# Kernel optimization log

Hardware: AMD Instinct MI355X
Metric: run time of the kernel (lower is better)

The kernel has to match this reference:

```python
import math
import jax, jax.numpy as jnp
import numpy as np

T, D = 1024, 7168
N = 128
A_Q, A_KV = 1536, 512
QK_NOPE, QK_ROPE, V_DIM = 128, 64, 128
QK_HEAD = QK_NOPE + QK_ROPE  # 192
PAD_H = 256                  # padded to multiple of 128 in attn_op
EPS = 1e-6
ROPE_THETA, FACTOR, ORIG_MAX = 10000.0, 40.0, 4096
BETA_FAST, BETA_SLOW = 32, 1


def _yarn_inv_freq():
    """DeepseekScalingRotaryEmbedding (yarn) inverse frequencies, static."""
    dim = QK_ROPE
    pos_freqs = ROPE_THETA ** (np.arange(0, dim, 2, dtype=np.float64) / dim)
    inv_extra = 1.0 / pos_freqs
    inv_inter = 1.0 / (FACTOR * pos_freqs)

    def corr_dim(n_rot):
        return dim * math.log(ORIG_MAX / (n_rot * 2 * math.pi)) / (2 * math.log(ROPE_THETA))

    low = max(math.floor(corr_dim(BETA_FAST)), 0)
    high = min(math.ceil(corr_dim(BETA_SLOW)), dim - 1)
    ramp = np.clip((np.arange(dim // 2, dtype=np.float64) - low) / max(high - low, 1e-3), 0.0, 1.0)
    mask = 1.0 - ramp  # 1 -> extrapolation, 0 -> interpolation
    inv = inv_inter * (1.0 - mask) + inv_extra * mask
    return jnp.asarray(inv, dtype=jnp.float32)

_INV_FREQ = _yarn_inv_freq()
# mscale ratio: yarn_get_mscale(FACTOR, mscale)/yarn_get_mscale(FACTOR, mscale_all_dim) == 1.0
_MSCALE = 1.0


def _apply_rope(positions, x):
    # x: [T, N, QK_ROPE], split (rotate-half) ordering
    ang = positions[:, None].astype(jnp.float32) * _INV_FREQ[None, :]  # [T, 32]
    cos = (jnp.cos(ang) * _MSCALE)[:, None, :]
    sin = (jnp.sin(ang) * _MSCALE)[:, None, :]
    x1, x2 = x[..., : QK_ROPE // 2], x[..., QK_ROPE // 2:]
    return jnp.concatenate([x1 * cos - x2 * sin, x2 * cos + x1 * sin], axis=-1)


def _rms_norm(x, scale):
    var = jnp.mean(x * x, axis=-1, keepdims=True)
    return x * jax.lax.rsqrt(var + EPS) * scale


def setup_inputs() -> dict:
    key = jax.random.key(0)
    ks = jax.random.split(key, 6)
    s = 0.02
    return {
        "x": jax.random.normal(ks[0], (T, D), jnp.float32),
        "positions": jnp.arange(T, dtype=jnp.int32),
        "w_q_down": jax.random.normal(ks[1], (D, A_Q), jnp.float32) * s,
        "q_norm_scale": jnp.ones((A_Q,), jnp.float32),
        "w_q_up": jax.random.normal(ks[2], (A_Q, N, QK_HEAD), jnp.float32) * s,
        "w_kv_down": jax.random.normal(ks[3], (D, A_KV + QK_ROPE), jnp.float32) * s,
        "kv_norm_scale": jnp.ones((A_KV,), jnp.float32),
        "w_kv_up": jax.random.normal(ks[4], (A_KV, N, QK_NOPE + V_DIM), jnp.float32) * s,
        "w_o": jax.random.normal(ks[5], (N, V_DIM, D), jnp.float32) * s,
    }


def reference(x, positions, w_q_down, q_norm_scale, w_q_up, w_kv_down,
              kv_norm_scale, w_kv_up, w_o):
    # ---- q path: down-proj -> RMSNorm -> up-proj -> split RoPE ----
    q_TA = jnp.einsum('td,da->ta', x, w_q_down)
    q_TA = _rms_norm(q_TA, q_norm_scale)
    q_TNH = jnp.einsum('ta,anh->tnh', q_TA, w_q_up)
    q_rope = _apply_rope(positions, q_TNH[..., QK_NOPE:])
    q_TNH = jnp.concatenate([q_TNH[..., :QK_NOPE], q_rope], axis=-1)
    q_TNH = q_TNH * (QK_HEAD ** -0.5)

    # ---- kv path: down-proj -> (rope slice | RMSNorm latent -> up-proj) ----
    kv_SA = jnp.einsum('sd,da->sa', x, w_kv_down)
    k_rope = _apply_rope(positions, kv_SA[..., A_KV:][:, None, :])  # [S,1,64]
    k_rope = jnp.broadcast_to(k_rope, (T, N, QK_ROPE))
    c_SA = _rms_norm(kv_SA[..., :A_KV], kv_norm_scale)
    kv_nope = jnp.einsum('sa,anh->snh', c_SA, w_kv_up)
    k_SNH = jnp.concatenate([kv_nope[..., :QK_NOPE], k_rope], axis=-1)
    v_SNH = kv_nope[..., QK_NOPE:]

    # ---- attention (prefill, causal); zero-pad of head dim does not change dots,
    # but sm_scale uses the PADDED dim (256) as in the original attn_op ----
    sm_scale = PAD_H ** -0.5
    logits = jnp.einsum('tnh,snh->nts', q_TNH, k_SNH) * sm_scale
    t_idx = jnp.arange(T)
    causal = t_idx[:, None] >= t_idx[None, :]  # [T, S]
    logits = jnp.where(causal[None, :, :], logits, jnp.float32(-1e30))
    probs = jax.nn.softmax(logits, axis=-1)
    out_TNH = jnp.einsum('nts,snh->tnh', probs, v_SNH)

    # ---- output projection ----
    o_TD = jnp.einsum('tnh,nhd->td', out_TNH, w_o)
    return o_TD
```

## Files before the change

### kernel.cpp

```cpp
#include <hip/hip_runtime.h>
#include <hip/hip_bf16.h>
#include <math.h>

typedef __attribute__((ext_vector_type(4))) float f32x4;
typedef __attribute__((ext_vector_type(8))) short bf16x8;
typedef __attribute__((ext_vector_type(4))) short bf16x4;

static __device__ __forceinline__ float bf2f(short u){
  unsigned int i = ((unsigned int)(unsigned short)u) << 16;
  return __builtin_bit_cast(float, i);
}
static __device__ __forceinline__ short f2bf(float f){
  unsigned int u = __builtin_bit_cast(unsigned int, f);
  u += 0x7FFFu + ((u >> 16) & 1u);
  return (short)(u >> 16);
}

#define GLD16(g, l) __builtin_amdgcn_global_load_lds(                         \
    (const __attribute__((address_space(1))) void*)(g),                       \
    (__attribute__((address_space(3))) void*)(l), 16, 0, 0)

template<typename CT, int SPLITS>
__global__ __launch_bounds__(512, 2) void gemm256(const short* __restrict__ A,
                                                  const short* __restrict__ BT,
                                                  CT* __restrict__ C,
                                                  float* __restrict__ P,
                                                  int M, int N, int K)
{
  extern __shared__ __align__(16) char smem[];
  const int tid = threadIdx.x;
  const int w = tid >> 6, lane = tid & 63;
  const int wm = w >> 2, wn = w & 3;
  const int g = lane >> 4, l16 = lane & 15;

  const int per_z = gridDim.x * gridDim.y;
  const int F = (blockIdx.z * gridDim.y + blockIdx.y) * gridDim.x + blockIdx.x;
  const int nwgF = per_z * gridDim.z;
  const int cpxF = nwgF >> 3;
  const int T = (F & 7) * cpxF + (F >> 3);
  const int zz = T / per_z, tt = T % per_z;
  const int m0 = (tt & 3) * 256;
  const int n0 = (tt >> 2) * 256;

  const int Ks   = K / SPLITS;
  const int kbeg = zz * Ks;
  const int NT   = Ks >> 5;

  const int gg = (lane & 3) ^ ((lane >> 2) & 3) ^ ((lane >> 4) & 1);
  const short* aSrc[2]; const short* bSrc[2];
  int ldsOff[2];
  #pragma unroll
  for (int j = 0; j < 2; j++){
    int r = (w + j*8)*16 + (lane >> 2);
    aSrc[j] = A  + (size_t)(m0 + r) * K + kbeg + gg*8;
    bSrc[j] = BT + (size_t)(n0 + r) * K + kbeg + gg*8;
    ldsOff[j] = (w + j*8) * 1024;
  }

  const int sw = ((g ^ (l16 & 3) ^ ((l16 >> 2) & 1)) << 4);

  f32x4 acc[8][4];
  #pragma unroll
  for (int i = 0; i < 8; i++)
    #pragma unroll
    for (int j = 0; j < 4; j++) acc[i][j] = (f32x4){0.f,0.f,0.f,0.f};

  auto stage = [&](int b, int t){
    const int koff = t * 32;
    char* dst = smem + b * 32768;
    #pragma unroll
    for (int j = 0; j < 2; j++){
      GLD16(aSrc[j] + koff, dst + ldsOff[j]);
      GLD16(bSrc[j] + koff, dst + 16384 + ldsOff[j]);
    }
  };

  auto wait_pub = [&](int ahead){
    if (ahead >= 3)      asm volatile("s_waitcnt vmcnt(8)" ::: "memory");
    else if (ahead == 2) asm volatile("s_waitcnt vmcnt(4)" ::: "memory");
    else                 asm volatile("s_waitcnt vmcnt(0)" ::: "memory");
    __builtin_amdgcn_s_barrier();
    asm volatile("" ::: "memory");
  };

  stage(0, 0);
  if (NT > 1) stage(1, 1);
  if (NT > 2) stage(2, 2);
  wait_pub(NT - 1 >= 2 ? (NT > 2 ? 3 : 2) : 1);

  const int arow = wm*128 + l16;
  const int brow = wn*64  + l16;

  for (int t = 0; t < NT; t++){
    const int sl = t & 3;
    if (t + 3 < NT) stage((t + 3) & 3, t + 3);

    const char* base = smem + sl * 32768;
    bf16x8 a[8], bb[4];
    #pragma unroll
    for (int mi = 0; mi < 8; mi++)
      a[mi] = *reinterpret_cast<const bf16x8*>(base + (arow + mi*16)*64 + sw);
    #pragma unroll
    for (int ni = 0; ni < 4; ni++)
      bb[ni] = *reinterpret_cast<const bf16x8*>(base + 16384 + (brow + ni*16)*64 + sw);

    __builtin_amdgcn_s_setprio(1);
    #pragma unroll
    for (int mi = 0; mi < 8; mi++)
      #pragma unroll
      for (int ni = 0; ni < 4; ni++)
        acc[mi][ni] = __builtin_amdgcn_mfma_f32_16x16x32_bf16(a[mi], bb[ni], acc[mi][ni], 0, 0, 0);
    __builtin_amdgcn_s_setprio(0);

    wait_pub(NT - 1 - t);
  }

  #pragma unroll
  for (int mi = 0; mi < 8; mi++){
    int row = m0 + wm*128 + mi*16 + g*4;
    #pragma unroll
    for (int ni = 0; ni < 4; ni++){
      int col = n0 + wn*64 + ni*16 + l16;
      #pragma unroll
      for (int r = 0; r < 4; r++){
        if constexpr (SPLITS > 1){
          P[(size_t)zz*M*N + (size_t)(row+r)*N + col] = acc[mi][ni][r];
        } else if constexpr (sizeof(CT) == 4){
          C[(size_t)(row+r)*N + col] = acc[mi][ni][r];
        } else {
          C[(size_t)(row+r)*N + col] = f2bf(acc[mi][ni][r]);
        }
      }
    }
  }
}

template<typename CT, int SPLITS>
__global__ __launch_bounds__(256) void gemm_bt(const short* __restrict__ A,
                                               const short* __restrict__ BT,
                                               CT* __restrict__ C,
                                               float* __restrict__ P,
                                               int M, int N, int K)
{
  __shared__ __align__(16) short As[2][128*32];
  __shared__ __align__(16) short Bs[2][128*32];
  const int tid = threadIdx.x;
  const int f   = blockIdx.y * 8 + blockIdx.x;
  const int nwg = 8 * gridDim.y;
  const int cpx = nwg >> 3;
  const int t   = (f & 7) * cpx + (f >> 3);
  const int m0  = (t & 7) * 128;
  const int n0  = (t >> 3) * 128;
  const int w = tid >> 6, lane = tid & 63;
  const int wr = w >> 1, wc = w & 1;
  const int g = lane >> 4, l16 = lane & 15;

  const int Ks   = K / SPLITS;
  const int kbeg = blockIdx.z * Ks;
  const int kend = kbeg + Ks;

  const int sr = lane >> 2;
  const int kc = (lane & 3) << 3;
  const int arow0 = m0 + w*16 + sr;
  const int arow1 = m0 + (w+4)*16 + sr;
  int brow0 = n0 + w*16 + sr;      if (brow0 >= N) brow0 = N - 1;
  int brow1 = n0 + (w+4)*16 + sr;  if (brow1 >= N) brow1 = N - 1;
  const short* aG0 = A  + (size_t)arow0 * K + kc;
  const short* aG1 = A  + (size_t)arow1 * K + kc;
  const short* bG0 = BT + (size_t)brow0 * K + kc;
  const short* bG1 = BT + (size_t)brow1 * K + kc;
  char* aL = (char*)As;
  char* bL = (char*)Bs;

  auto stage = [&](int buf, int k0){
    char* ab = aL + buf*8192;
    char* bb = bL + buf*8192;
    GLD16(aG0 + k0, ab + (w  )*1024);
    GLD16(aG1 + k0, ab + (w+4)*1024);
    GLD16(bG0 + k0, bb + (w  )*1024);
    GLD16(bG1 + k0, bb + (w+4)*1024);
  };

  f32x4 acc[4][4];
  #pragma unroll
  for (int i=0;i<4;i++)
    #pragma unroll
    for (int j=0;j<4;j++) acc[i][j] = (f32x4){0.f,0.f,0.f,0.f};

  stage(0, kbeg);
  __syncthreads();

  int cur = 0;
  for (int k0 = kbeg; k0 < kend; k0 += 32){
    if (k0 + 32 < kend) stage(cur ^ 1, k0 + 32);

    const char* ar = aL + cur*8192;
    const char* br = bL + cur*8192;
    bf16x8 af[4], bfm[4];
    #pragma unroll
    for (int mi=0;mi<4;mi++){
      int row = wr*64 + mi*16 + l16;
      af[mi] = *reinterpret_cast<const bf16x8*>(ar + row*64 + g*16);
    }
    #pragma unroll
    for (int ni=0;ni<4;ni++){
      int row = wc*64 + ni*16 + l16;
      bfm[ni] = *reinterpret_cast<const bf16x8*>(br + row*64 + g*16);
    }
    #pragma unroll
    for (int mi=0;mi<4;mi++)
      #pragma unroll
      for (int ni=0;ni<4;ni++)
        acc[mi][ni] = __builtin_amdgcn_mfma_f32_16x16x32_bf16(af[mi], bfm[ni], acc[mi][ni], 0, 0, 0);

    __syncthreads();
    cur ^= 1;
  }

  #pragma unroll
  for (int mi=0;mi<4;mi++){
    int row = m0 + wr*64 + mi*16 + g*4;
    #pragma unroll
    for (int ni=0;ni<4;ni++){
      int col = n0 + wc*64 + ni*16 + l16;
      if (col < N){
        #pragma unroll
        for (int r=0;r<4;r++){
          if constexpr (SPLITS > 1){
            P[(size_t)blockIdx.z*M*N + (size_t)(row+r)*N + col] = acc[mi][ni][r];
          } else if constexpr (sizeof(CT) == 4){
            C[(size_t)(row+r)*N + col] = acc[mi][ni][r];
          } else {
            C[(size_t)(row+r)*N + col] = f2bf(acc[mi][ni][r]);
          }
        }
      }
    }
  }
}

template<int NP>
__global__ __launch_bounds__(256) void reduceN(const float* __restrict__ p,
                                               float* __restrict__ out,
                                               int n4, int mn4)
{
  int i = blockIdx.x * 256 + threadIdx.x;
  const int stride = gridDim.x * 256;
  for (; i < n4; i += stride){
    f32x4 s = reinterpret_cast<const f32x4*>(p)[i];
    #pragma unroll
    for (int z = 1; z < NP; z++)
      s = s + reinterpret_cast<const f32x4*>(p)[(size_t)z*mn4 + i];
    reinterpret_cast<f32x4*>(out)[i] = s;
  }
}

__global__ __launch_bounds__(256) void transpose_f32_bf16(const float* __restrict__ src,
                                                          short* __restrict__ dst,
                                                          int R, int C)
{
  __shared__ float tl[64][68];
  const int tid = threadIdx.x;
  const int r0 = blockIdx.y * 64, c0 = blockIdx.x * 64;
  {
    const int lr = tid >> 4, lc = (tid & 15) << 2;
    #pragma unroll
    for (int p = 0; p < 4; p++){
      int row = p*16 + lr;
      f32x4 v = *reinterpret_cast<const f32x4*>(src + (size_t)(r0+row)*C + c0 + lc);
      *reinterpret_cast<f32x4*>(&tl[row][lc]) = v;
    }
  }
  __syncthreads();
  {
    const int n = tid >> 2, ks = (tid & 3) << 4;
    short tmp[16];
    #pragma unroll
    for (int j = 0; j < 16; j++) tmp[j] = f2bf(tl[ks + j][n]);
    short* d = dst + (size_t)(c0+n)*R + r0 + ks;
    *reinterpret_cast<bf16x8*>(d)     = *reinterpret_cast<bf16x8*>(&tmp[0]);
    *reinterpret_cast<bf16x8*>(d + 8) = *reinterpret_cast<bf16x8*>(&tmp[8]);
  }
}

__global__ __launch_bounds__(256) void conv_f32_bf16(const float* __restrict__ src,
                                                     short* __restrict__ dst, int n4)
{
  int i = blockIdx.x * 256 + threadIdx.x;
  const int stride = gridDim.x * 256;
  for (; i < n4; i += stride){
    f32x4 v = reinterpret_cast<const f32x4*>(src)[i];
    bf16x4 h; h[0]=f2bf(v[0]); h[1]=f2bf(v[1]); h[2]=f2bf(v[2]); h[3]=f2bf(v[3]);
    reinterpret_cast<bf16x4*>(dst)[i] = h;
  }
}

__global__ __launch_bounds__(256) void mla_rmsnorm_bf(const float* __restrict__ dc,
                                                      const float* __restrict__ scale,
                                                      short* __restrict__ out)
{
  const int t = blockIdx.x;
  const float* row = dc + (size_t)t * 2112;
  float ss = 0.f;
  for (int i = threadIdx.x; i < 1536; i += 256){ float v = row[i]; ss += v*v; }
  #pragma unroll
  for (int off = 32; off >= 1; off >>= 1) ss += __shfl_xor(ss, off);
  __shared__ float red[4];
  if ((threadIdx.x & 63) == 0) red[threadIdx.x >> 6] = ss;
  __syncthreads();
  ss = red[0] + red[1] + red[2] + red[3];
  const float rs = 1.0f / sqrtf(ss / 1536.f + 1e-6f);
  for (int i = threadIdx.x; i < 1536; i += 256)
    out[(size_t)t*1536 + i] = f2bf(row[i] * rs * scale[i]);
}

__device__ __forceinline__ void yarn_cs(int pos, int j, float& c, float& s){
  const double dim = 64.0;
  double pf = pow(10000.0, (2.0*(double)j)/dim);
  double inv_extra = 1.0/pf;
  double inv_inter = inv_extra/40.0;
  double lo = floor(dim*log(4096.0/(32.0*2.0*M_PI))/(2.0*log(10000.0)));
  double hi = ceil (dim*log(4096.0/(       2.0*M_PI))/(2.0*log(10000.0)));
  if (lo < 0.0) lo = 0.0;
  if (hi > dim - 1.0) hi = dim - 1.0;
  double denom = hi - lo; if (denom < 0.001) denom = 0.001;
  double ramp = ((double)j - lo)/denom;
  ramp = ramp < 0.0 ? 0.0 : (ramp > 1.0 ? 1.0 : ramp);
  double mask = 1.0 - ramp;
  float invf = (float)(inv_inter*(1.0 - mask) + inv_extra*mask);
  float ang = (float)pos * invf;
  c = cosf(ang); s = sinf(ang);
}

__global__ __launch_bounds__(256) void mla_rope_q(short* __restrict__ qb,
                                                  const int* __restrict__ positions)
{
  const int t = blockIdx.x;
  __shared__ float cs[32], sn[32];
  if (threadIdx.x < 32){
    float c, s; yarn_cs(positions[t], threadIdx.x, c, s);
    cs[threadIdx.x] = c; sn[threadIdx.x] = s;
  }
  __syncthreads();
  const float f = 0.004510548978043951f;
  short* row = qb + (size_t)t * 24576;
  for (int idx = threadIdx.x; idx < 128*160; idx += 256){
    int n = idx / 160, e = idx % 160;
    short* p = row + n*192;
    if (e < 128){
      p[e] = f2bf(bf2f(p[e]) * f);
    } else {
      int j = e - 128;
      float x1 = bf2f(p[128+j]), x2 = bf2f(p[160+j]);
      p[128+j] = f2bf((x1*cs[j] - x2*sn[j]) * f);
      p[160+j] = f2bf((x2*cs[j] + x1*sn[j]) * f);
    }
  }
}

__global__ __launch_bounds__(256) void mla_kv_post(const float* __restrict__ dc,
                                                   const float* __restrict__ scale,
                                                   const int* __restrict__ positions,
                                                   short* __restrict__ cbuf,
                                                   short* __restrict__ krope)
{
  const int t = blockIdx.x;
  const float* row = dc + (size_t)t * 2112 + 1536;
  float ss = 0.f;
  for (int i = threadIdx.x; i < 512; i += 256){ float v = row[i]; ss += v*v; }
  #pragma unroll
  for (int off = 32; off >= 1; off >>= 1) ss += __shfl_xor(ss, off);
  __shared__ float red[4];
  if ((threadIdx.x & 63) == 0) red[threadIdx.x >> 6] = ss;
  __syncthreads();
  ss = red[0] + red[1] + red[2] + red[3];
  const float rs = 1.0f / sqrtf(ss / 512.f + 1e-6f);
  for (int i = threadIdx.x; i < 512; i += 256)
    cbuf[(size_t)t*512 + i] = f2bf(row[i] * rs * scale[i]);
  if (threadIdx.x < 32){
    int j = threadIdx.x;
    float c, s; yarn_cs(positions[t], j, c, s);
    float x1 = row[512 + j], x2 = row[544 + j];
    krope[(size_t)t*64 + j]      = f2bf(x1*c - x2*s);
    krope[(size_t)t*64 + 32 + j] = f2bf(x2*c + x1*s);
  }
}

__global__ __launch_bounds__(512) void mla_attn2(const short* __restrict__ qb,
                                                 const short* __restrict__ kvup,
                                                 const short* __restrict__ krope,
                                                 short* __restrict__ attn_out)
{
  const int f = blockIdx.x;
  const int xcd = f & 7, pos = f >> 3;
  const int n  = xcd*16 + (pos >> 2);
  const int pair = pos & 3;
  const int tid = threadIdx.x, w = tid >> 6, lane = tid & 63;
  const int g = lane >> 4, l16 = lane & 15;

  __shared__ __align__(16) short Klds[64*192];
  __shared__ __align__(16) short Vlds[128*64];
  __shared__ __align__(16) short Plds[8][16*64];
  char* KB = (char*)Klds; char* VB = (char*)Vlds; char* PB = (char*)Plds[w];

  bf16x8 kpre[3];
  bf16x4 vpreA[2], vpreB[2];

  int kS[3], kHB[3];
  #pragma unroll
  for (int c=0;c<3;c++){
    int lin = c*512 + tid;
    kS[c] = lin / 24; kHB[c] = (lin % 24) * 8;
  }
  int vV4[2], vS2[2];
  #pragma unroll
  for (int c=0;c<2;c++){
    int lin = c*512 + tid;
    vV4[c] = (lin & 31) << 2; vS2[c] = (lin >> 5) << 1;
  }

  auto stage_load = [&](int S0){
    #pragma unroll
    for (int c=0;c<3;c++){
      const short* src = (kHB[c] < 128)
        ? kvup  + (size_t)(S0 + kS[c])*32768 + n*256 + kHB[c]
        : krope + (size_t)(S0 + kS[c])*64 + (kHB[c]-128);
      kpre[c] = *reinterpret_cast<const bf16x8*>(src);
    }
    #pragma unroll
    for (int c=0;c<2;c++){
      vpreA[c] = *reinterpret_cast<const bf16x4*>(kvup + (size_t)(S0 + vS2[c]  )*32768 + n*256 + 128 + vV4[c]);
      vpreB[c] = *reinterpret_cast<const bf16x4*>(kvup + (size_t)(S0 + vS2[c]+1)*32768 + n*256 + 128 + vV4[c]);
    }
  };
  auto stage_write = [&](){
    #pragma unroll
    for (int c=0;c<3;c++){
      unsigned byte = (unsigned)(kS[c]*384 + kHB[c]*2) ^ ((unsigned)(kS[c]&7)<<4);
      *reinterpret_cast<bf16x8*>(KB + byte) = kpre[c];
    }
    #pragma unroll
    for (int c=0;c<2;c++){
      const int pos2 = vS2[c] * 2;
      #pragma unroll
      for (int i=0;i<4;i++){
        int v = vV4[c] + i;
        unsigned byte = (unsigned)(v*128 + ((((pos2 >> 4) ^ (v & 7)) << 4) | (pos2 & 15)));
        unsigned pk = (unsigned)(unsigned short)vpreA[c][i] |
                      ((unsigned)(unsigned short)vpreB[c][i] << 16);
        *reinterpret_cast<unsigned*>(VB + byte) = pk;
      }
    }
  };

  stage_load(0);
  stage_write();
  __syncthreads();

  #pragma unroll
  for (int p = 0; p < 2; p++){
    const int qtl = p ? (7 - pair) : pair;
    const int t0 = qtl * 128;
    const int last = 2*qtl + 1;

    bf16x8 qf[6];
    {
      const size_t qrow = (size_t)(t0 + w*16 + l16) * 24576 + (size_t)n * 192;
      #pragma unroll
      for (int c=0;c<6;c++)
        qf[c] = *reinterpret_cast<const bf16x8*>(qb + qrow + c*32 + g*8);
    }
    f32x4 o[8];
    #pragma unroll
    for (int i=0;i<8;i++) o[i] = (f32x4){0.f,0.f,0.f,0.f};
    float m[4], l[4];
    #pragma unroll
    for (int r=0;r<4;r++){ m[r] = -1e30f; l[r] = 0.f; }

    for (int sb = 0; sb <= last; sb++){
      const bool more = (sb < last) || (p == 0);
      if (more) stage_load((sb < last) ? (sb+1)*64 : 0);

      f32x4 S[4];
      __builtin_amdgcn_s_setprio(1);
      #pragma unroll
      for (int st=0; st<4; st++){
        f32x4 sacc = (f32x4){0.f,0.f,0.f,0.f};
        int srow = st*16 + l16;
        #pragma unroll
        for (int c=0;c<6;c++){
          unsigned byte = (unsigned)(srow*384 + c*64 + g*16) ^ ((unsigned)(srow&7)<<4);
          bf16x8 kf = *reinterpret_cast<const bf16x8*>(KB + byte);
          sacc = __builtin_amdgcn_mfma_f32_16x16x32_bf16(qf[c], kf, sacc, 0, 0, 0);
        }
        S[st] = sacc;
      }
      __builtin_amdgcn_s_setprio(0);

      if (sb >= 2*qtl){
        #pragma unroll
        for (int st=0;st<4;st++){
          int sg = sb*64 + st*16 + l16;
          #pragma unroll
          for (int r=0;r<4;r++){
            int qg = t0 + w*16 + g*4 + r;
            if (sg > qg) S[st][r] = -1e30f;
          }
        }
      }
      float alpha[4];
      #pragma unroll
      for (int r=0;r<4;r++){
        float mx = fmaxf(fmaxf(S[0][r],S[1][r]), fmaxf(S[2][r],S[3][r]));
        #pragma unroll
        for (int off=8; off>=1; off>>=1) mx = fmaxf(mx, __shfl_xor(mx, off));
        float mnew = fmaxf(m[r], mx);
        alpha[r] = __expf(m[r] - mnew);
        m[r] = mnew;
        l[r] *= alpha[r];
      }
      #pragma unroll
      for (int st=0;st<4;st++)
        #pragma unroll
        for (int r=0;r<4;r++)
          S[st][r] = __expf(S[st][r] - m[r]);
      #pragma unroll
      for (int r=0;r<4;r++){
        float sum = S[0][r]+S[1][r]+S[2][r]+S[3][r];
        #pragma unroll
        for (int off=8; off>=1; off>>=1) sum += __shfl_xor(sum, off);
        l[r] += sum;
      }
      #pragma unroll
      for (int vt=0; vt<8; vt++)
        #pragma unroll
        for (int r=0;r<4;r++) o[vt][r] *= alpha[r];

      #pragma unroll
      for (int st=0;st<4;st++){
        #pragma unroll
        for (int r=0;r<4;r++){
          int qrow = g*4 + r, scol = st*16 + l16;
          unsigned byte = (unsigned)(qrow*128 + scol*2) ^ ((unsigned)(qrow&7)<<4);
          *reinterpret_cast<short*>(PB + byte) = f2bf(S[st][r]);
        }
      }
      bf16x8 pf[2];
      #pragma unroll
      for (int c=0;c<2;c++){
        unsigned byte = (unsigned)(l16*128 + (c*32 + g*8)*2) ^ ((unsigned)(l16&7)<<4);
        pf[c] = *reinterpret_cast<const bf16x8*>(PB + byte);
      }
      __builtin_amdgcn_s_setprio(1);
      #pragma unroll
      for (int vt=0; vt<8; vt++){
        #pragma unroll
        for (int c=0;c<2;c++){
          int vrow = vt*16 + l16;
          unsigned byte = (unsigned)(vrow*128 + ((unsigned)(c*64 + g*16) ^ ((unsigned)(vrow&7)<<4)));
          bf16x8 vf = *reinterpret_cast<const bf16x8*>(VB + byte);
          o[vt] = __builtin_amdgcn_mfma_f32_16x16x32_bf16(pf[c], vf, o[vt], 0, 0, 0);
        }
      }
      __builtin_amdgcn_s_setprio(0);

      if (more){
        __syncthreads();
        stage_write();
        __syncthreads();
      }
    }

    #pragma unroll
    for (int r=0;r<4;r++){
      float inv = 1.f / l[r];
      int t = t0 + w*16 + g*4 + r;
      #pragma unroll
      for (int vt=0;vt<8;vt++){
        int v = vt*16 + l16;
        attn_out[(size_t)t*16384 + n*128 + v] = f2bf(o[vt][r] * inv);
      }
    }
  }
}

extern "C" void kernel_launch(void* const* d_in, const int* in_sizes, int n_in,
                              void* d_out, int out_size, void* d_ws, size_t ws_size,
                              hipStream_t stream) {
  const float* x            = (const float*)d_in[0];
  const int*   positions    = (const int*)  d_in[1];
  const float* w_q_down     = (const float*)d_in[2];
  const float* q_norm_scale = (const float*)d_in[3];
  const float* w_q_up       = (const float*)d_in[4];
  const float* w_kv_down    = (const float*)d_in[5];
  const float* kv_norm_scale= (const float*)d_in[6];
  const float* w_kv_up      = (const float*)d_in[7];
  const float* w_o          = (const float*)d_in[8];

  char* p = (char*)d_ws;
  short* xbf   = (short*)p; p += (size_t)1024*7168*2;
  short* wdT   = (short*)p; p += (size_t)2112*7168*2;
  short* wquT  = (short*)p; p += (size_t)24576*1536*2;
  short* wkuT  = (short*)p; p += (size_t)32768*512*2;
  short* woT   = (short*)p; p += (size_t)7168*16384*2;
  float* downC = (float*)p; p += (size_t)1024*2112*4;
  short* qAbf  = (short*)p; p += (size_t)1024*1536*2;
  short* q_b   = (short*)p; p += (size_t)1024*24576*2;
  short* cbuf  = (short*)p; p += (size_t)1024*512*2;
  short* krope = (short*)p; p += (size_t)1024*64*2;
  short* kvup  = (short*)p; p += (size_t)1024*32768*2;
  short* attn_o= (short*)p; p += (size_t)1024*16384*2;

  float* pDown = (float*)q_b;
  float* pWo   = (float*)d_ws;

  hipFuncSetAttribute(reinterpret_cast<const void*>(&gemm256<short,1>),
                      hipFuncAttributeMaxDynamicSharedMemorySize, 131072);
  hipFuncSetAttribute(reinterpret_cast<const void*>(&gemm256<float,2>),
                      hipFuncAttributeMaxDynamicSharedMemorySize, 131072);

  dim3 blk(256);
  conv_f32_bf16<<<2048, blk, 0, stream>>>(x, xbf, 1024*7168/4);
  transpose_f32_bf16<<<dim3(24, 112),  blk, 0, stream>>>(w_q_down,  wdT,                     7168, 1536);
  transpose_f32_bf16<<<dim3(9, 112),   blk, 0, stream>>>(w_kv_down, wdT + (size_t)1536*7168, 7168, 576);
  transpose_f32_bf16<<<dim3(384, 24),  blk, 0, stream>>>(w_q_up,    wquT,                    1536, 24576);
  transpose_f32_bf16<<<dim3(512, 8),   blk, 0, stream>>>(w_kv_up,   wkuT,                    512,  32768);
  transpose_f32_bf16<<<dim3(112, 256), blk, 0, stream>>>(w_o,       woT,                     16384, 7168);

  gemm_bt<float, 4><<<dim3(8, 17, 4), blk, 0, stream>>>(xbf, wdT, (float*)nullptr, pDown, 1024, 2112, 7168);
  reduceN<4><<<1024, blk, 0, stream>>>(pDown, downC, 1024*2112/4, 1024*2112/4);
  mla_rmsnorm_bf<<<1024, blk, 0, stream>>>(downC, q_norm_scale, qAbf);
  mla_kv_post<<<1024, blk, 0, stream>>>(downC, kv_norm_scale, positions, cbuf, krope);

  gemm256<short, 1><<<dim3(4, 96), dim3(512), 131072, stream>>>(qAbf, wquT, q_b, nullptr, 1024, 24576, 1536);
  mla_rope_q<<<1024, blk, 0, stream>>>(q_b, positions);
  gemm256<short, 1><<<dim3(4, 128), dim3(512), 131072, stream>>>(cbuf, wkuT, kvup, nullptr, 1024, 32768, 512);

  mla_attn2<<<512, dim3(512), 0, stream>>>(q_b, kvup, krope, attn_o);

  gemm256<float, 2><<<dim3(4, 28, 2), dim3(512), 131072, stream>>>(attn_o, woT, (float*)nullptr, pWo, 1024, 7168, 16384);
  reduceN<2><<<2048, blk, 0, stream>>>(pWo, (float*)d_out, 1024*7168/4, 1024*7168/4);
}
```

Before: 891.7 us.

## Fuse q RoPE into up-proj epilogue, merge norm kernels, use 256-tile split-K down-proj

Folds the q RoPE rotation and softmax prescale into the q up-projection GEMM epilogue, which removes a separate read-modify-write pass over the large q buffer. The down-projection moves from the 128-tile gemm_bt to the 256-tile gemm256 with 7-way split-K, using an XCD mapping that handles tile counts not divisible by 8. The two RMSNorm/post kernels are merged into one, and cos/sin values are precomputed once into a table. The cost is a 7-way partial reduction and a split-K buffer moved onto kvup, plus divergent epilogue branches per wave.

New measurement: 920.4 us. 3.2% more time.

```diff
diff --git a/kernel.cpp b/kernel.cpp
--- a/kernel.cpp
+++ b/kernel.cpp
@@ -20,11 +20,12 @@
     (const __attribute__((address_space(1))) void*)(g),                       \
     (__attribute__((address_space(3))) void*)(l), 16, 0, 0)
 
-template<typename CT, int SPLITS>
+template<typename CT, int SPLITS, bool ROPE>
 __global__ __launch_bounds__(512, 2) void gemm256(const short* __restrict__ A,
                                                   const short* __restrict__ BT,
                                                   CT* __restrict__ C,
                                                   float* __restrict__ P,
+                                                  const float* __restrict__ csn,
                                                   int M, int N, int K)
 {
   extern __shared__ __align__(16) char smem[];
@@ -36,8 +37,10 @@
   const int per_z = gridDim.x * gridDim.y;
   const int F = (blockIdx.z * gridDim.y + blockIdx.y) * gridDim.x + blockIdx.x;
   const int nwgF = per_z * gridDim.z;
-  const int cpxF = nwgF >> 3;
-  const int T = (F & 7) * cpxF + (F >> 3);
+  const int qq = nwgF >> 3, rr = nwgF & 7;
+  const int xcd = F & 7;
+  const int base = (xcd < rr) ? xcd * (qq + 1) : rr * (qq + 1) + (xcd - rr) * qq;
+  const int T = base + (F >> 3);
   const int zz = T / per_z, tt = T % per_z;
   const int m0 = (tt & 3) * 256;
   const int n0 = (tt >> 2) * 256;
@@ -52,8 +55,9 @@
   #pragma unroll
   for (int j = 0; j < 2; j++){
     int r = (w + j*8)*16 + (lane >> 2);
+    int br = n0 + r; if (br >= N) br = N - 1;
     aSrc[j] = A  + (size_t)(m0 + r) * K + kbeg + gg*8;
-    bSrc[j] = BT + (size_t)(n0 + r) * K + kbeg + gg*8;
+    bSrc[j] = BT + (size_t)br      * K + kbeg + gg*8;
     ldsOff[j] = (w + j*8) * 1024;
   }
 
@@ -95,14 +99,14 @@
     const int sl = t & 3;
     if (t + 3 < NT) stage((t + 3) & 3, t + 3);
 
-    const char* base = smem + sl * 32768;
+    const char* base2 = smem + sl * 32768;
     bf16x8 a[8], bb[4];
     #pragma unroll
     for (int mi = 0; mi < 8; mi++)
-      a[mi] = *reinterpret_cast<const bf16x8*>(base + (arow + mi*16)*64 + sw);
+      a[mi] = *reinterpret_cast<const bf16x8*>(base2 + (arow + mi*16)*64 + sw);
     #pragma unroll
     for (int ni = 0; ni < 4; ni++)
-      bb[ni] = *reinterpret_cast<const bf16x8*>(base + 16384 + (brow + ni*16)*64 + sw);
+      bb[ni] = *reinterpret_cast<const bf16x8*>(base2 + 16384 + (brow + ni*16)*64 + sw);
 
     __builtin_amdgcn_s_setprio(1);
     #pragma unroll
@@ -115,123 +119,53 @@
     wait_pub(NT - 1 - t);
   }
 
-  #pragma unroll
-  for (int mi = 0; mi < 8; mi++){
-    int row = m0 + wm*128 + mi*16 + g*4;
-    #pragma unroll
-    for (int ni = 0; ni < 4; ni++){
-      int col = n0 + wn*64 + ni*16 + l16;
+  if constexpr (ROPE) {
+    const float fsc = 0.004510548978043951f;
+    const int W = (n0 >> 6) + wn;
+    const bool ropew = (W % 3) == 2;
+    #pragma unroll
+    for (int mi = 0; mi < 8; mi++){
+      int row = m0 + wm*128 + mi*16 + g*4;
       #pragma unroll
       for (int r = 0; r < 4; r++){
-        if constexpr (SPLITS > 1){
-          P[(size_t)zz*M*N + (size_t)(row+r)*N + col] = acc[mi][ni][r];
-        } else if constexpr (sizeof(CT) == 4){
-          C[(size_t)(row+r)*N + col] = acc[mi][ni][r];
+        int t = row + r;
+        if (!ropew){
+          #pragma unroll
+          for (int ni = 0; ni < 4; ni++){
+            int col = n0 + wn*64 + ni*16 + l16;
+            C[(size_t)t*N + col] = f2bf(acc[mi][ni][r] * fsc);
+          }
         } else {
-          C[(size_t)(row+r)*N + col] = f2bf(acc[mi][ni][r]);
+          #pragma unroll
+          for (int ni = 0; ni < 2; ni++){
+            int j = ni*16 + l16;
+            float c = csn[((size_t)t*32 + j)*2];
+            float s = csn[((size_t)t*32 + j)*2 + 1];
+            float x1 = acc[mi][ni][r], x2 = acc[mi][ni+2][r];
+            int col = n0 + wn*64 + ni*16 + l16;
+            C[(size_t)t*N + col]      = f2bf((x1*c - x2*s) * fsc);
+            C[(size_t)t*N + col + 32] = f2bf((x2*c + x1*s) * fsc);
+          }
         }
       }
     }
-  }
-}
-
-template<typename CT, int SPLITS>
-__global__ __launch_bounds__(256) void gemm_bt(const short* __restrict__ A,
-                                               const short* __restrict__ BT,
-                                               CT* __restrict__ C,
-                                               float* __restrict__ P,
-                                               int M, int N, int K)
-{
-  __shared__ __align__(16) short As[2][128*32];
-  __shared__ __align__(16) short Bs[2][128*32];
-  const int tid = threadIdx.x;
-  const int f   = blockIdx.y * 8 + blockIdx.x;
-  const int nwg = 8 * gridDim.y;
-  const int cpx = nwg >> 3;
-  const int t   = (f & 7) * cpx + (f >> 3);
-  const int m0  = (t & 7) * 128;
-  const int n0  = (t >> 3) * 128;
-  const int w = tid >> 6, lane = tid & 63;
-  const int wr = w >> 1, wc = w & 1;
-  const int g = lane >> 4, l16 = lane & 15;
-
-  const int Ks   = K / SPLITS;
-  const int kbeg = blockIdx.z * Ks;
-  const int kend = kbeg + Ks;
-
-  const int sr = lane >> 2;
-  const int kc = (lane & 3) << 3;
-  const int arow0 = m0 + w*16 + sr;
-  const int arow1 = m0 + (w+4)*16 + sr;
-  int brow0 = n0 + w*16 + sr;      if (brow0 >= N) brow0 = N - 1;
-  int brow1 = n0 + (w+4)*16 + sr;  if (brow1 >= N) brow1 = N - 1;
-  const short* aG0 = A  + (size_t)arow0 * K + kc;
-  const short* aG1 = A  + (size_t)arow1 * K + kc;
-  const short* bG0 = BT + (size_t)brow0 * K + kc;
-  const short* bG1 = BT + (size_t)brow1 * K + kc;
-  char* aL = (char*)As;
-  char* bL = (char*)Bs;
-
-  auto stage = [&](int buf, int k0){
-    char* ab = aL + buf*8192;
-    char* bb = bL + buf*8192;
-    GLD16(aG0 + k0, ab + (w  )*1024);
-    GLD16(aG1 + k0, ab + (w+4)*1024);
-    GLD16(bG0 + k0, bb + (w  )*1024);
-    GLD16(bG1 + k0, bb + (w+4)*1024);
-  };
-
-  f32x4 acc[4][4];
-  #pragma unroll
-  for (int i=0;i<4;i++)
-    #pragma unroll
-    for (int j=0;j<4;j++) acc[i][j] = (f32x4){0.f,0.f,0.f,0.f};
-
-  stage(0, kbeg);
-  __syncthreads();
-
-  int cur = 0;
-  for (int k0 = kbeg; k0 < kend; k0 += 32){
-    if (k0 + 32 < kend) stage(cur ^ 1, k0 + 32);
-
-    const char* ar = aL + cur*8192;
-    const char* br = bL + cur*8192;
-    bf16x8 af[4], bfm[4];
-    #pragma unroll
-    for (int mi=0;mi<4;mi++){
-      int row = wr*64 + mi*16 + l16;
-      af[mi] = *reinterpret_cast<const bf16x8*>(ar + row*64 + g*16);
-    }
-    #pragma unroll
-    for (int ni=0;ni<4;ni++){
-      int row = wc*64 + ni*16 + l16;
-      bfm[ni] = *reinterpret_cast<const bf16x8*>(br + row*64 + g*16);
-    }
-    #pragma unroll
-    for (int mi=0;mi<4;mi++)
-      #pragma unroll
-      for (int ni=0;ni<4;ni++)
-        acc[mi][ni] = __builtin_amdgcn_mfma_f32_16x16x32_bf16(af[mi], bfm[ni], acc[mi][ni], 0, 0, 0);
-
-    __syncthreads();
-    cur ^= 1;
-  }
-
-  #pragma unroll
-  for (int mi=0;mi<4;mi++){
-    int row = m0 + wr*64 + mi*16 + g*4;
-    #pragma unroll
-    for (int ni=0;ni<4;ni++){
-      int col = n0 + wc*64 + ni*16 + l16;
-      if (col < N){
-        #pragma unroll
-        for (int r=0;r<4;r++){
-          if constexpr (SPLITS > 1){
-            P[(size_t)blockIdx.z*M*N + (size_t)(row+r)*N + col] = acc[mi][ni][r];
-          } else if constexpr (sizeof(CT) == 4){
-            C[(size_t)(row+r)*N + col] = acc[mi][ni][r];
-          } else {
-            C[(size_t)(row+r)*N + col] = f2bf(acc[mi][ni][r]);
+  } else {
+    #pragma unroll
+    for (int mi = 0; mi < 8; mi++){
+      int row = m0 + wm*128 + mi*16 + g*4;
+      #pragma unroll
+      for (int ni = 0; ni < 4; ni++){
+        int col = n0 + wn*64 + ni*16 + l16;
+        if (col < N){
+          #pragma unroll
+          for (int r = 0; r < 4; r++){
+            if constexpr (SPLITS > 1){
+              P[(size_t)zz*M*N + (size_t)(row+r)*N + col] = acc[mi][ni][r];
+            } else if constexpr (sizeof(CT) == 4){
+              C[(size_t)(row+r)*N + col] = acc[mi][ni][r];
+            } else {
+              C[(size_t)(row+r)*N + col] = f2bf(acc[mi][ni][r]);
+            }
           }
         }
       }
@@ -293,25 +227,6 @@
     bf16x4 h; h[0]=f2bf(v[0]); h[1]=f2bf(v[1]); h[2]=f2bf(v[2]); h[3]=f2bf(v[3]);
     reinterpret_cast<bf16x4*>(dst)[i] = h;
   }
-}
-
-__global__ __launch_bounds__(256) void mla_rmsnorm_bf(const float* __restrict__ dc,
-                                                      const float* __restrict__ scale,
-                                                      short* __restrict__ out)
-{
-  const int t = blockIdx.x;
-  const float* row = dc + (size_t)t * 2112;
-  float ss = 0.f;
-  for (int i = threadIdx.x; i < 1536; i += 256){ float v = row[i]; ss += v*v; }
-  #pragma unroll
-  for (int off = 32; off >= 1; off >>= 1) ss += __shfl_xor(ss, off);
-  __shared__ float red[4];
-  if ((threadIdx.x & 63) == 0) red[threadIdx.x >> 6] = ss;
-  __syncthreads();
-  ss = red[0] + red[1] + red[2] + red[3];
-  const float rs = 1.0f / sqrtf(ss / 1536.f + 1e-6f);
-  for (int i = threadIdx.x; i < 1536; i += 256)
-    out[(size_t)t*1536 + i] = f2bf(row[i] * rs * scale[i]);
 }
 
 __device__ __forceinline__ void yarn_cs(int pos, int j, float& c, float& s){
@@ -332,55 +247,47 @@
   c = cosf(ang); s = sinf(ang);
 }
 
-__global__ __launch_bounds__(256) void mla_rope_q(short* __restrict__ qb,
-                                                  const int* __restrict__ positions)
+__global__ __launch_bounds__(64) void mla_csn(const int* __restrict__ positions,
+                                              float* __restrict__ csn)
+{
+  const int t = blockIdx.x, j = threadIdx.x;
+  if (j < 32){
+    float c, s; yarn_cs(positions[t], j, c, s);
+    csn[((size_t)t*32 + j)*2]     = c;
+    csn[((size_t)t*32 + j)*2 + 1] = s;
+  }
+}
+
+__global__ __launch_bounds__(256) void mla_post(const float* __restrict__ dc,
+                                                const float* __restrict__ qs,
+                                                const float* __restrict__ kvs,
+                                                const float* __restrict__ csn,
+                                                short* __restrict__ qAbf,
+                                                short* __restrict__ cbuf,
+                                                short* __restrict__ krope)
 {
   const int t = blockIdx.x;
-  __shared__ float cs[32], sn[32];
-  if (threadIdx.x < 32){
-    float c, s; yarn_cs(positions[t], threadIdx.x, c, s);
-    cs[threadIdx.x] = c; sn[threadIdx.x] = s;
-  }
+  const float* row = dc + (size_t)t * 2112;
+  float s1 = 0.f, s2 = 0.f;
+  for (int i = threadIdx.x; i < 1536; i += 256){ float v = row[i]; s1 += v*v; }
+  for (int i = threadIdx.x; i < 512;  i += 256){ float v = row[1536+i]; s2 += v*v; }
+  #pragma unroll
+  for (int off = 32; off >= 1; off >>= 1){ s1 += __shfl_xor(s1, off); s2 += __shfl_xor(s2, off); }
+  __shared__ float red[8];
+  if ((threadIdx.x & 63) == 0){ red[threadIdx.x >> 6] = s1; red[4 + (threadIdx.x >> 6)] = s2; }
   __syncthreads();
-  const float f = 0.004510548978043951f;
-  short* row = qb + (size_t)t * 24576;
-  for (int idx = threadIdx.x; idx < 128*160; idx += 256){
-    int n = idx / 160, e = idx % 160;
-    short* p = row + n*192;
-    if (e < 128){
-      p[e] = f2bf(bf2f(p[e]) * f);
-    } else {
-      int j = e - 128;
-      float x1 = bf2f(p[128+j]), x2 = bf2f(p[160+j]);
-      p[128+j] = f2bf((x1*cs[j] - x2*sn[j]) * f);
-      p[160+j] = f2bf((x2*cs[j] + x1*sn[j]) * f);
-    }
-  }
-}
-
-__global__ __launch_bounds__(256) void mla_kv_post(const float* __restrict__ dc,
-                                                   const float* __restrict__ scale,
-                                                   const int* __restrict__ positions,
-                                                   short* __restrict__ cbuf,
-                                                   short* __restrict__ krope)
-{
-  const int t = blockIdx.x;
-  const float* row = dc + (size_t)t * 2112 + 1536;
-  float ss = 0.f;
-  for (int i = threadIdx.x; i < 512; i += 256){ float v = row[i]; ss += v*v; }
-  #pragma unroll
-  for (int off = 32; off >= 1; off >>= 1) ss += __shfl_xor(ss, off);
-  __shared__ float red[4];
-  if ((threadIdx.x & 63) == 0) red[threadIdx.x >> 6] = ss;
-  __syncthreads();
-  ss = red[0] + red[1] + red[2] + red[3];
-  const float rs = 1.0f / sqrtf(ss / 512.f + 1e-6f);
+  s1 = red[0]+red[1]+red[2]+red[3];
+  s2 = red[4]+red[5]+red[6]+red[7];
+  const float rs1 = 1.0f / sqrtf(s1 / 1536.f + 1e-6f);
+  const float rs2 = 1.0f / sqrtf(s2 / 512.f  + 1e-6f);
+  for (int i = threadIdx.x; i < 1536; i += 256)
+    qAbf[(size_t)t*1536 + i] = f2bf(row[i] * rs1 * qs[i]);
   for (int i = threadIdx.x; i < 512; i += 256)
-    cbuf[(size_t)t*512 + i] = f2bf(row[i] * rs * scale[i]);
+    cbuf[(size_t)t*512 + i] = f2bf(row[1536+i] * rs2 * kvs[i]);
   if (threadIdx.x < 32){
     int j = threadIdx.x;
-    float c, s; yarn_cs(positions[t], j, c, s);
-    float x1 = row[512 + j], x2 = row[544 + j];
+    float c = csn[((size_t)t*32 + j)*2], s = csn[((size_t)t*32 + j)*2 + 1];
+    float x1 = row[2048 + j], x2 = row[2080 + j];
     krope[(size_t)t*64 + j]      = f2bf(x1*c - x2*s);
     krope[(size_t)t*64 + 32 + j] = f2bf(x2*c + x1*s);
   }
@@ -610,13 +517,18 @@
   short* krope = (short*)p; p += (size_t)1024*64*2;
   short* kvup  = (short*)p; p += (size_t)1024*32768*2;
   short* attn_o= (short*)p; p += (size_t)1024*16384*2;
-
-  float* pDown = (float*)q_b;
+  float* csn   = (float*)p; p += (size_t)1024*32*2*4;
+
+  float* pDown = (float*)kvup;
   float* pWo   = (float*)d_ws;
 
-  hipFuncSetAttribute(reinterpret_cast<const void*>(&gemm256<short,1>),
+  hipFuncSetAttribute(reinterpret_cast<const void*>(&gemm256<short,1,false>),
                       hipFuncAttributeMaxDynamicSharedMemorySize, 131072);
-  hipFuncSetAttribute(reinterpret_cast<const void*>(&gemm256<float,2>),
+  hipFuncSetAttribute(reinterpret_cast<const void*>(&gemm256<short,1,true>),
+                      hipFuncAttributeMaxDynamicSharedMemorySize, 131072);
+  hipFuncSetAttribute(reinterpret_cast<const void*>(&gemm256<float,2,false>),
+                      hipFuncAttributeMaxDynamicSharedMemorySize, 131072);
+  hipFuncSetAttribute(reinterpret_cast<const void*>(&gemm256<float,7,false>),
                       hipFuncAttributeMaxDynamicSharedMemorySize, 131072);
 
   dim3 blk(256);
@@ -626,18 +538,21 @@
   transpose_f32_bf16<<<dim3(384, 24),  blk, 0, stream>>>(w_q_up,    wquT,                    1536, 24576);
   transpose_f32_bf16<<<dim3(512, 8),   blk, 0, stream>>>(w_kv_up,   wkuT,                    512,  32768);
   transpose_f32_bf16<<<dim3(112, 256), blk, 0, stream>>>(w_o,       woT,                     16384, 7168);
-
-  gemm_bt<float, 4><<<dim3(8, 17, 4), blk, 0, stream>>>(xbf, wdT, (float*)nullptr, pDown, 1024, 2112, 7168);
-  reduceN<4><<<1024, blk, 0, stream>>>(pDown, downC, 1024*2112/4, 1024*2112/4);
-  mla_rmsnorm_bf<<<1024, blk, 0, stream>>>(downC, q_norm_scale, qAbf);
-  mla_kv_post<<<1024, blk, 0, stream>>>(downC, kv_norm_scale, positions, cbuf, krope);
-
-  gemm256<short, 1><<<dim3(4, 96), dim3(512), 131072, stream>>>(qAbf, wquT, q_b, nullptr, 1024, 24576, 1536);
-  mla_rope_q<<<1024, blk, 0, stream>>>(q_b, positions);
-  gemm256<short, 1><<<dim3(4, 128), dim3(512), 131072, stream>>>(cbuf, wkuT, kvup, nullptr, 1024, 32768, 512);
+  mla_csn<<<1024, 64, 0, stream>>>(positions, csn);
+
+  gemm256<float, 7, false><<<dim3(4, 9, 7), dim3(512), 131072, stream>>>(
+      xbf, wdT, (float*)nullptr, pDown, nullptr, 1024, 2112, 7168);
+  reduceN<7><<<1024, blk, 0, stream>>>(pDown, downC, 1024*2112/4, 1024*2112/4);
+  mla_post<<<1024, blk, 0, stream>>>(downC, q_norm_scale, kv_norm_scale, csn, qAbf, cbuf, krope);
+
+  gemm256<short, 1, true><<<dim3(4, 96), dim3(512), 131072, stream>>>(
+      qAbf, wquT, q_b, nullptr, csn, 1024, 24576, 1536);
+  gemm256<short, 1, false><<<dim3(4, 128), dim3(512), 131072, stream>>>(
+      cbuf, wkuT, kvup, nullptr, nullptr, 1024, 32768, 512);
 
   mla_attn2<<<512, dim3(512), 0, stream>>>(q_b, kvup, krope, attn_o);
 
-  gemm256<float, 2><<<dim3(4, 28, 2), dim3(512), 131072, stream>>>(attn_o, woT, (float*)nullptr, pWo, 1024, 7168, 16384);
+  gemm256<float, 2, false><<<dim3(4, 28, 2), dim3(512), 131072, stream>>>(
+      attn_o, woT, (float*)nullptr, pWo, nullptr, 1024, 7168, 16384);
   reduceN<2><<<2048, blk, 0, stream>>>(pWo, (float*)d_out, 1024*7168/4, 1024*7168/4);
 }
```
